# Optimization experiments

Hardware: AMD Instinct MI355X
Metric: run time of the kernel (lower is better)

The kernel has to match this reference:

```python
import jax, jax.numpy as jnp
import numpy as np

HDIM = 32
U_DIM = 8
HID = 128
T = 65536
DYN_GAIN = 0.02
STATE_DAMP = 0.1
H_CLIP = 5.0
DT = np.float32(5.0 / 60.0)  # 5 minutes in hours


def _xavier(key, shape):
    fan_in, fan_out = shape[0], shape[1]
    limit = np.sqrt(6.0 / (fan_in + fan_out)).astype(np.float32)
    return jax.random.uniform(key, shape, jnp.float32, -limit, limit)


def setup_inputs() -> dict:
    key = jax.random.key(0)
    ks = jax.random.split(key, 8)
    U = jax.random.normal(ks[0], (T, U_DIM), jnp.float32)
    params = {
        "U": U,
        "h0": jnp.zeros((1, HDIM), jnp.float32),
        "W1": _xavier(ks[1], (HDIM + U_DIM, HID)), "b1": jnp.zeros((HID,), jnp.float32),
        "W2": _xavier(ks[2], (HID, HID)), "b2": jnp.zeros((HID,), jnp.float32),
        "W3": _xavier(ks[3], (HID, HDIM)), "b3": jnp.zeros((HDIM,), jnp.float32),
        "Wd": _xavier(ks[4], (HDIM, 1)), "bd": jnp.zeros((1,), jnp.float32),
        "Wt": _xavier(ks[5], (HDIM, 1)), "bt": jnp.zeros((1,), jnp.float32),
        "Wc": _xavier(ks[6], (HDIM, 1)), "bc": jnp.zeros((1,), jnp.float32),
    }
    return params


def reference(U, h0, W1, b1, W2, b2, W3, b3, Wd, bd, Wt, bt, Wc, bc):
    dt = jnp.float32(DT)

    def dyn(h, u):
        # h: [1, HDIM], u: [1, U_DIM]
        x = jnp.concatenate([h, u], axis=-1)
        z = jax.nn.silu(x @ W1 + b1)
        z = jax.nn.silu(z @ W2 + b2)
        drift = z @ W3 + b3
        return DYN_GAIN * drift - STATE_DAMP * h

    def step(h, u_t):
        u = u_t[None, :]  # [1, U_DIM]
        # readout of current state (before the RK4 step, as in the torch loop)
        d = (h @ Wd + bd)[..., 0]  # [1]
        t = (h @ Wt + bt)[..., 0]
        c = (h @ Wc + bc)[..., 0]
        k1 = dyn(h, u)
        k2 = dyn(h + 0.5 * dt * k1, u)
        k3 = dyn(h + 0.5 * dt * k2, u)
        k4 = dyn(h + dt * k3, u)
        h_next = h + dt / 6.0 * (k1 + 2.0 * k2 + 2.0 * k3 + k4)
        h_next = jnp.nan_to_num(h_next, nan=0.0, posinf=0.0, neginf=0.0)
        h_next = jnp.clip(jnp.tanh(h_next), -H_CLIP, H_CLIP)
        return h_next, (d, t, c)

    h_last, (ds, ts, cs) = jax.lax.scan(step, h0, U)
    # ds/ts/cs: [T, 1] -> [T]
    return ds.squeeze(-1), ts.squeeze(-1), cs.squeeze(-1), h_last
```

## Files before the change

### kernel.cpp

```cpp
#include <hip/hip_runtime.h>
#include <math.h>


constexpr int T_STEPS = 65536;
constexpr int HD  = 32;
constexpr int HID = 128;

typedef float v2f __attribute__((ext_vector_type(2)));

__device__ __forceinline__ v2f fma2(v2f a, v2f b, v2f c) {
    return __builtin_elementwise_fma(a, b, c);
}

__device__ __forceinline__ float silu_f(float a) {
    return a / (1.0f + __expf(-a));
}

__device__ __forceinline__ void wg_barrier() {
    asm volatile("s_waitcnt lgkmcnt(0)" ::: "memory");
    __builtin_amdgcn_s_barrier();
    asm volatile("" ::: "memory");
}

__global__ __launch_bounds__(128, 1)
void node_scan(const float* __restrict__ U,
               const float* __restrict__ h0,
               const float* __restrict__ W1, const float* __restrict__ b1,
               const float* __restrict__ W2, const float* __restrict__ b2,
               const float* __restrict__ W3, const float* __restrict__ b3,
               const float* __restrict__ Wd, const float* __restrict__ bd,
               const float* __restrict__ Wt, const float* __restrict__ bt,
               const float* __restrict__ Wc, const float* __restrict__ bc,
               float* __restrict__ out)
{
    const int tid = threadIdx.x;
    const int j   = tid;
    const int l   = tid & 63;
    const int m   = tid & 31;
    const int seg = tid >> 5;
    const int wv  = tid >> 6;

    __shared__ __align__(16) float xbuf[HD];
    __shared__ __align__(16) float z1buf[HID];
    __shared__ __align__(16) float z2slot[HID];
    __shared__ __align__(16) float pex[2 * HID];
    __shared__ __align__(16) float pb2[64];

    v2f w1p[20];
#pragma unroll
    for (int i = 0; i < 20; ++i) {
        w1p[i].x = W1[(2 * i) * HID + j];
        w1p[i].y = W1[(2 * i + 1) * HID + j];
    }
    const float b1r = b1[j];

    v2f w2a[32], w2b[32];
#pragma unroll
    for (int kp = 0; kp < 32; ++kp) {
        const int k = wv * 64 + 2 * kp;
        w2a[kp].x = W2[k * HID + l];
        w2a[kp].y = W2[(k + 1) * HID + l];
        w2b[kp].x = W2[k * HID + l + 64];
        w2b[kp].y = W2[(k + 1) * HID + l + 64];
    }
    const float b2a = b2[l], b2b = b2[l + 64];

    v2f w3p[16];
#pragma unroll
    for (int i = 0; i < 16; ++i) {
        w3p[i].x = W3[(seg * 16 + i) * HD + m];
        w3p[i].y = W3[(seg * 16 + i + 64) * HD + m];
    }
    const float b3r = b3[m];

    const float whr = (wv == 0) ? Wd[m] : Wt[m];
    const float wcr = Wc[m];
    const float bd0 = bd[0], bt0 = bt[0], bc0 = bc[0];

    float hm   = h0[m];
    float xm   = hm;
    float kacc = 0.0f;

    const float DT  = 5.0f / 60.0f;
    const float HDT = 0.5f * DT;
    const float W6  = DT / 6.0f;

    float4 ua = *(const float4*)(U);
    float4 ub = *(const float4*)(U + 4);

    xbuf[m] = xm;
    wg_barrier();

    for (int t = 0; t < T_STEPS; ++t) {
        const int tn = (t + 1 < T_STEPS) ? (t + 1) : t;
        const float4 na = *(const float4*)(U + tn * 8);
        const float4 nb = *(const float4*)(U + tn * 8 + 4);

        {
            float p  = hm * whr;
            float pc = hm * wcr;
            p += __shfl_xor(p, 16);  pc += __shfl_xor(pc, 16);
            p += __shfl_xor(p, 8);   pc += __shfl_xor(pc, 8);
            p += __shfl_xor(p, 4);   pc += __shfl_xor(pc, 4);
            p += __shfl_xor(p, 2);   pc += __shfl_xor(pc, 2);
            p += __shfl_xor(p, 1);   pc += __shfl_xor(pc, 1);
            if (tid == 0)  { out[t] = p + bd0; out[2 * T_STEPS + t] = pc + bc0; }
            if (tid == 64) { out[T_STEPS + t] = p + bt0; }
        }

        float upj;
        {
            v2f u0; u0.x = ua.x; u0.y = ua.y;
            v2f u1; u1.x = ua.z; u1.y = ua.w;
            v2f u2; u2.x = ub.x; u2.y = ub.y;
            v2f u3; u3.x = ub.z; u3.y = ub.w;
            v2f up = {b1r, 0.0f};
            up = fma2(u0, w1p[16], up);
            up = fma2(u1, w1p[17], up);
            up = fma2(u2, w1p[18], up);
            up = fma2(u3, w1p[19], up);
            upj = up.x + up.y;
        }

#pragma unroll
        for (int st = 0; st < 4; ++st) {
            v2f a0 = {upj, 0.0f}, a1 = {0.0f, 0.0f};
            const float4* xv = (const float4*)xbuf;
#pragma unroll
            for (int i4 = 0; i4 < 8; ++i4) {
                const float4 v = xv[i4];
                v2f lo; lo.x = v.x; lo.y = v.y;
                v2f hi; hi.x = v.z; hi.y = v.w;
                a0 = fma2(lo, w1p[2 * i4],     a0);
                a1 = fma2(hi, w1p[2 * i4 + 1], a1);
            }
            const v2f as = a0 + a1;
            z1buf[j] = silu_f(as.x + as.y);
            __builtin_amdgcn_wave_barrier();

            v2f aA0 = {0.0f, 0.0f}, aA1 = {0.0f, 0.0f};
            v2f aB0 = {0.0f, 0.0f}, aB1 = {0.0f, 0.0f};
            const float4* z1v = (const float4*)(z1buf + wv * 64);
#pragma unroll
            for (int i4 = 0; i4 < 16; ++i4) {
                const float4 v = z1v[i4];
                v2f lo; lo.x = v.x; lo.y = v.y;
                v2f hi; hi.x = v.z; hi.y = v.w;
                aA0 = fma2(lo, w2a[2 * i4],     aA0);
                aA1 = fma2(hi, w2a[2 * i4 + 1], aA1);
                aB0 = fma2(lo, w2b[2 * i4],     aB0);
                aB1 = fma2(hi, w2b[2 * i4 + 1], aB1);
            }
            const v2f sA = aA0 + aA1;
            const v2f sB = aB0 + aB1;
            float2 mine;
            mine.x = sA.x + sA.y;
            mine.y = sB.x + sB.y;
            ((float2*)pex)[wv * 64 + l] = mine;
            wg_barrier();

            const float2 po = ((const float2*)pex)[(1 ^ wv) * 64 + l];
            const float z2A = silu_f(mine.x + po.x + b2a);
            const float z2B = silu_f(mine.y + po.y + b2b);
            float2 zs; zs.x = z2A; zs.y = z2B;
            ((float2*)z2slot)[l] = zs;
            __builtin_amdgcn_wave_barrier();

            v2f p0 = {0.0f, 0.0f}, p1 = {0.0f, 0.0f};
            const float4* z2v = (const float4*)(z2slot + seg * 32);
#pragma unroll
            for (int i4 = 0; i4 < 8; ++i4) {
                const float4 v = z2v[i4];
                v2f lo; lo.x = v.x; lo.y = v.y;
                v2f hi; hi.x = v.z; hi.y = v.w;
                p0 = fma2(lo, w3p[2 * i4],     p0);
                p1 = fma2(hi, w3p[2 * i4 + 1], p1);
            }
            const v2f ps = p0 + p1;
            float pr = ps.x + ps.y;
            pr += __shfl_xor(pr, 32);
            pb2[2 * m + wv] = pr;
            wg_barrier();

            {
                const float2 pp = ((const float2*)pb2)[m];
                const float drift = (pp.x + pp.y) + b3r;
                const float k = 0.02f * drift - 0.1f * xm;
                if (st == 0)      { kacc = k;           xm = hm + HDT * k; }
                else if (st == 1) { kacc += 2.0f * k;   xm = hm + HDT * k; }
                else if (st == 2) { kacc += 2.0f * k;   xm = hm + DT  * k; }
                else {
                    kacc += k;
                    float hn = hm + W6 * kacc;
                    if (!isfinite(hn)) hn = 0.0f;
                    hn = tanhf(hn);
                    hn = fminf(fmaxf(hn, -5.0f), 5.0f);
                    hm = hn; xm = hn;
                }
                xbuf[m] = xm;
            }
            __builtin_amdgcn_wave_barrier();
        }
        ua = na; ub = nb;
    }

    if (tid < HD) out[3 * T_STEPS + tid] = hm;
}

extern "C" void kernel_launch(void* const* d_in, const int* in_sizes, int n_in,
                              void* d_out, int out_size, void* d_ws, size_t ws_size,
                              hipStream_t stream) {
    const float* U  = (const float*)d_in[0];
    const float* h0 = (const float*)d_in[1];
    const float* W1 = (const float*)d_in[2];
    const float* b1 = (const float*)d_in[3];
    const float* W2 = (const float*)d_in[4];
    const float* b2 = (const float*)d_in[5];
    const float* W3 = (const float*)d_in[6];
    const float* b3 = (const float*)d_in[7];
    const float* Wd = (const float*)d_in[8];
    const float* bd = (const float*)d_in[9];
    const float* Wt = (const float*)d_in[10];
    const float* bt = (const float*)d_in[11];
    const float* Wc = (const float*)d_in[12];
    const float* bc = (const float*)d_in[13];
    float* out = (float*)d_out;

    node_scan<<<1, 128, 0, stream>>>(U, h0, W1, b1, W2, b2, W3, b3,
                                     Wd, bd, Wt, bt, Wc, bc, out);
}
```

Before: 235.9 ms.

## Make each wave compute full layer-3 drift redundantly to drop a barrier per stage

Each wave now computes the full 128-wide layer-3 reduction using 64 W3 register pairs, so the drift no longer needs a cross-wave exchange. This removes one workgroup barrier per RK stage. The layer-2 exchange buffer is double-buffered so the remaining single barrier is enough. The U-projection weights move from registers to LDS to free registers. The cost is twice the layer-3 FMAs per wave, more register pressure, and extra LDS reads for the U term.

```diff
diff --git a/kernel.cpp b/kernel.cpp
--- a/kernel.cpp
+++ b/kernel.cpp
@@ -37,18 +37,21 @@
     const int j   = tid;
     const int l   = tid & 63;
     const int m   = tid & 31;
-    const int seg = tid >> 5;
+    const int kh  = (tid >> 5) & 1;
     const int wv  = tid >> 6;
 
     __shared__ __align__(16) float xbuf[HD];
     __shared__ __align__(16) float z1buf[HID];
     __shared__ __align__(16) float z2slot[HID];
-    __shared__ __align__(16) float pex[2 * HID];
-    __shared__ __align__(16) float pb2[64];
-
-    v2f w1p[20];
-#pragma unroll
-    for (int i = 0; i < 20; ++i) {
+    __shared__ __align__(16) float pexbuf[2][2 * HID];
+    __shared__ __align__(16) float upart[8 * HID];
+
+#pragma unroll
+    for (int i = 0; i < 8; ++i) upart[i * HID + j] = W1[(32 + i) * HID + j];
+
+    v2f w1p[16];
+#pragma unroll
+    for (int i = 0; i < 16; ++i) {
         w1p[i].x = W1[(2 * i) * HID + j];
         w1p[i].y = W1[(2 * i + 1) * HID + j];
     }
@@ -65,11 +68,11 @@
     }
     const float b2a = b2[l], b2b = b2[l + 64];
 
-    v2f w3p[16];
-#pragma unroll
-    for (int i = 0; i < 16; ++i) {
-        w3p[i].x = W3[(seg * 16 + i) * HD + m];
-        w3p[i].y = W3[(seg * 16 + i + 64) * HD + m];
+    v2f w3p[32];
+#pragma unroll
+    for (int i = 0; i < 32; ++i) {
+        w3p[i].x = W3[(kh * 32 + i) * HD + m];
+        w3p[i].y = W3[(kh * 32 + i + 64) * HD + m];
     }
     const float b3r = b3[m];
 
@@ -108,22 +111,18 @@
             if (tid == 64) { out[T_STEPS + t] = p + bt0; }
         }
 
-        float upj;
+        float upj = b1r;
         {
-            v2f u0; u0.x = ua.x; u0.y = ua.y;
-            v2f u1; u1.x = ua.z; u1.y = ua.w;
-            v2f u2; u2.x = ub.x; u2.y = ub.y;
-            v2f u3; u3.x = ub.z; u3.y = ub.w;
-            v2f up = {b1r, 0.0f};
-            up = fma2(u0, w1p[16], up);
-            up = fma2(u1, w1p[17], up);
-            up = fma2(u2, w1p[18], up);
-            up = fma2(u3, w1p[19], up);
-            upj = up.x + up.y;
+            const float uu[8] = {ua.x, ua.y, ua.z, ua.w, ub.x, ub.y, ub.z, ub.w};
+#pragma unroll
+            for (int i = 0; i < 8; ++i)
+                upj = fmaf(uu[i], upart[i * HID + j], upj);
         }
 
 #pragma unroll
         for (int st = 0; st < 4; ++st) {
+            const int p = st & 1;
+
             v2f a0 = {upj, 0.0f}, a1 = {0.0f, 0.0f};
             const float4* xv = (const float4*)xbuf;
 #pragma unroll
@@ -156,10 +155,10 @@
             float2 mine;
             mine.x = sA.x + sA.y;
             mine.y = sB.x + sB.y;
-            ((float2*)pex)[wv * 64 + l] = mine;
+            ((float2*)pexbuf[p])[wv * 64 + l] = mine;
             wg_barrier();
 
-            const float2 po = ((const float2*)pex)[(1 ^ wv) * 64 + l];
+            const float2 po = ((const float2*)pexbuf[p])[(1 ^ wv) * 64 + l];
             const float z2A = silu_f(mine.x + po.x + b2a);
             const float z2B = silu_f(mine.y + po.y + b2b);
             float2 zs; zs.x = z2A; zs.y = z2B;
@@ -167,38 +166,39 @@
             __builtin_amdgcn_wave_barrier();
 
             v2f p0 = {0.0f, 0.0f}, p1 = {0.0f, 0.0f};
-            const float4* z2v = (const float4*)(z2slot + seg * 32);
-#pragma unroll
-            for (int i4 = 0; i4 < 8; ++i4) {
+            v2f p2 = {0.0f, 0.0f}, p3 = {0.0f, 0.0f};
+            const float4* z2v = (const float4*)(z2slot + kh * 64);
+#pragma unroll
+            for (int i4 = 0; i4 < 16; ++i4) {
                 const float4 v = z2v[i4];
                 v2f lo; lo.x = v.x; lo.y = v.y;
                 v2f hi; hi.x = v.z; hi.y = v.w;
-                p0 = fma2(lo, w3p[2 * i4],     p0);
-                p1 = fma2(hi, w3p[2 * i4 + 1], p1);
-            }
-            const v2f ps = p0 + p1;
+                if (i4 & 1) {
+                    p2 = fma2(lo, w3p[2 * i4],     p2);
+                    p3 = fma2(hi, w3p[2 * i4 + 1], p3);
+                } else {
+                    p0 = fma2(lo, w3p[2 * i4],     p0);
+                    p1 = fma2(hi, w3p[2 * i4 + 1], p1);
+                }
+            }
+            const v2f ps = (p0 + p1) + (p2 + p3);
             float pr = ps.x + ps.y;
             pr += __shfl_xor(pr, 32);
-            pb2[2 * m + wv] = pr;
-            wg_barrier();
-
-            {
-                const float2 pp = ((const float2*)pb2)[m];
-                const float drift = (pp.x + pp.y) + b3r;
-                const float k = 0.02f * drift - 0.1f * xm;
-                if (st == 0)      { kacc = k;           xm = hm + HDT * k; }
-                else if (st == 1) { kacc += 2.0f * k;   xm = hm + HDT * k; }
-                else if (st == 2) { kacc += 2.0f * k;   xm = hm + DT  * k; }
-                else {
-                    kacc += k;
-                    float hn = hm + W6 * kacc;
-                    if (!isfinite(hn)) hn = 0.0f;
-                    hn = tanhf(hn);
-                    hn = fminf(fmaxf(hn, -5.0f), 5.0f);
-                    hm = hn; xm = hn;
-                }
-                xbuf[m] = xm;
-            }
+            const float drift = pr + b3r;
+
+            const float k = 0.02f * drift - 0.1f * xm;
+            if (st == 0)      { kacc = k;           xm = hm + HDT * k; }
+            else if (st == 1) { kacc += 2.0f * k;   xm = hm + HDT * k; }
+            else if (st == 2) { kacc += 2.0f * k;   xm = hm + DT  * k; }
+            else {
+                kacc += k;
+                float hn = hm + W6 * kacc;
+                if (!isfinite(hn)) hn = 0.0f;
+                hn = tanhf(hn);
+                hn = fminf(fmaxf(hn, -5.0f), 5.0f);
+                hm = hn; xm = hn;
+            }
+            xbuf[m] = xm;
             __builtin_amdgcn_wave_barrier();
         }
         ua = na; ub = nb;
```

Result: slower. 424.4 ms (+79.9%).
